# Kernel optimization log

Measured on AMD Instinct MI355X. Metric: run time of the kernel, lower is better.

The kernel has to match this reference:

```python
import jax, jax.numpy as jnp
import numpy as np

B, T, N_EMBD, HEAD = 4, 4096, 2048, 128


def setup_inputs() -> dict:
    key = jax.random.key(0)
    kx, kq, kk, kv = jax.random.split(key, 4)
    scale = 1.0 / np.sqrt(N_EMBD)
    return {
        "x": jax.random.normal(kx, (B, T, N_EMBD), dtype=jnp.float32),
        "Wq": jax.random.normal(kq, (N_EMBD, HEAD), dtype=jnp.float32) * scale,
        "Wk": jax.random.normal(kk, (N_EMBD, HEAD), dtype=jnp.float32) * scale,
        "Wv": jax.random.normal(kv, (N_EMBD, HEAD), dtype=jnp.float32) * scale,
    }


def reference(x, Wq, Wk, Wv):
    # q, k, v: [B, T, H]
    q = jnp.einsum("btn,nh->bth", x, Wq)
    k = jnp.einsum("btn,nh->bth", x, Wk)
    v = jnp.einsum("btn,nh->bth", x, Wv)
    scale = 1.0 / jnp.sqrt(jnp.asarray(HEAD, dtype=x.dtype))
    scores = jnp.einsum("bth,bsh->bts", q, k) * scale  # [B, T, T]
    causal = jnp.tril(jnp.ones((T, T), dtype=bool))
    scores = jnp.where(causal, scores, -jnp.inf)
    weights = jax.nn.softmax(scores, axis=-1)  # dropout p=0.0 -> identity
    return jnp.einsum("bts,bsh->bth", weights, v)
```

## Files before the change

kernel.cpp:

```cpp
#include <hip/hip_runtime.h>
#include <hip/hip_bf16.h>

#define B_SZ  4
#define T_SEQ 4096
#define NE    2048
#define HD    128
#define NROWS (B_SZ * T_SEQ)

typedef __attribute__((ext_vector_type(4))) float f32x4;
typedef __attribute__((ext_vector_type(8))) short s16x8;

__device__ __forceinline__ ushort f2bf(float f) {
    __hip_bfloat16 h = __float2bfloat16(f);
    return *reinterpret_cast<ushort*>(&h);
}
__device__ __forceinline__ unsigned int pk2(float a, float b) {
    return (unsigned int)f2bf(a) | ((unsigned int)f2bf(b) << 16);
}
__device__ __forceinline__ void gload_lds16(const void* g, void* l) {
    __builtin_amdgcn_global_load_lds(
        (const __attribute__((address_space(1))) unsigned int*)g,
        (__attribute__((address_space(3))) unsigned int*)l, 16, 0, 0);
}

__global__ __launch_bounds__(256) void wconv_kernel(
    const float* __restrict__ Wq, const float* __restrict__ Wk,
    const float* __restrict__ Wv, ushort* __restrict__ wt)
{
    __shared__ __align__(16) ushort tr[128][80];
    const int mat = blockIdx.y;
    const int k0  = blockIdx.x * 64;
    const float* W = (mat == 0) ? Wq : (mat == 1) ? Wk : Wv;
    const int tid = threadIdx.x;

    #pragma unroll
    for (int p = 0; p < 32; p++) {
        const int idx = p * 256 + tid;
        const int k = idx >> 7, h = idx & 127;
        tr[h][k] = f2bf(W[(size_t)(k0 + k) * HD + h]);
    }
    __syncthreads();
    const int h = tid >> 1, half = tid & 1;
    const uint4* src = (const uint4*)&tr[h][half * 32];
    uint4* dst = (uint4*)(wt + (size_t)(mat * HD + h) * NE + k0 + half * 32);
    #pragma unroll
    for (int j = 0; j < 4; j++) dst[j] = src[j];
}

__global__ __launch_bounds__(512) void qkv_kernel(
    const float* __restrict__ x, const ushort* __restrict__ wt,
    ushort* __restrict__ q_b, ushort* __restrict__ k_b, ushort* __restrict__ vt)
{
    __shared__ __align__(16) ushort xa[2][64][64];
    __shared__ __align__(16) ushort wb[2][384][64];

    const int tid  = threadIdx.x;
    const int wave = tid >> 6, lane = tid & 63;
    const int nn   = lane & 15, quad = lane >> 4;
    const int rows0 = blockIdx.x * 64;
    const int wr = (wave & 3) * 16;
    const int wc = (wave >> 2) * 192;

    f32x4 acc[12];
    #pragma unroll
    for (int nt = 0; nt < 12; nt++) acc[nt] = (f32x4){0.f, 0.f, 0.f, 0.f};

    const int srow = tid >> 3, skq = tid & 7;
    const float* xp = x + (size_t)(rows0 + srow) * NE + skq * 8;
    char* xw = (char*)&xa[0][srow][0] + ((skq * 16) ^ ((srow & 7) << 4));

    float4 xr0, xr1;
    auto load_x = [&](int kc) {
        xr0 = *(const float4*)(xp + kc);
        xr1 = *(const float4*)(xp + kc + 4);
    };
    auto write_x = [&](int buf) {
        uint4 w;
        w.x = pk2(xr0.x, xr0.y); w.y = pk2(xr0.z, xr0.w);
        w.z = pk2(xr1.x, xr1.y); w.w = pk2(xr1.z, xr1.w);
        *(uint4*)(xw + buf * 8192) = w;
    };

    const int row8 = lane >> 3, off16 = (lane & 7) * 16;
    const char* wsrc = (const char*)wt
        + (size_t)(wave * 48 + row8) * (NE * 2) + (off16 ^ (row8 << 4));
    char* wdst = (char*)&wb[0][wave * 48][0];

    auto stage_w = [&](int buf, int kc) {
        #pragma unroll
        for (int j = 0; j < 6; j++)
            gload_lds16(wsrc + (size_t)j * 8 * (NE * 2) + kc * 2,
                        wdst + buf * 49152 + j * 1024);
    };

    load_x(0);
    stage_w(0, 0);
    write_x(0);
    asm volatile("s_waitcnt vmcnt(0)" ::: "memory");
    __syncthreads();

    for (int t = 0; t < 32; t++) {
        const int kc = t * 64;
        const int cb = t & 1;
        if (t + 1 < 32) { load_x(kc + 64); stage_w(cb ^ 1, kc + 64); }
        #pragma unroll
        for (int ks = 0; ks < 2; ks++) {
            const int kb = ks * 64 + quad * 16;
            const s16x8 af = *(const s16x8*)((const char*)&xa[cb][wr + nn][0]
                                             + (kb ^ ((nn & 7) << 4)));
            #pragma unroll
            for (int nt = 0; nt < 12; nt++) {
                const int c = wc + nt * 16 + nn;
                const s16x8 bf = *(const s16x8*)((const char*)&wb[cb][c][0]
                                                 + (kb ^ ((nn & 7) << 4)));
                acc[nt] = __builtin_amdgcn_mfma_f32_16x16x32_bf16(af, bf, acc[nt], 0, 0, 0);
            }
        }
        if (t + 1 < 32) write_x(cb ^ 1);
        __syncthreads();
    }

    const float qscale = 0.08838834764831845f;
    #pragma unroll
    for (int nt = 0; nt < 12; nt++) {
        const int c = wc + nt * 16 + nn;
        #pragma unroll
        for (int r = 0; r < 4; r++) {
            const int grow = rows0 + wr + quad * 4 + r;
            const float val = acc[nt][r];
            if (c < 128)       q_b[(size_t)grow * HD + c] = f2bf(val * qscale);
            else if (c < 256)  k_b[(size_t)grow * HD + (c - 128)] = f2bf(val);
            else               vt[(size_t)(c - 256) * NROWS + grow] = f2bf(val);
        }
    }
}

__global__ __launch_bounds__(256) void attn_kernel(
    const ushort* __restrict__ q_b, const ushort* __restrict__ k_b,
    const ushort* __restrict__ vt, float* __restrict__ out)
{
    __shared__ __align__(16) char smem_raw[4 * 16 * 132 * 4];
    float (*o_smem)[16][132] = reinterpret_cast<float (*)[16][132]>(smem_raw);
    ushort (*pT)[68]         = reinterpret_cast<ushort (*)[68]>(smem_raw);
    __shared__ float l_smem[4][16];

    const int bid = blockIdx.x;
    const int xcd = bid & 7;
    const int b   = xcd >> 1;
    const int qi  = 255 - (((bid >> 3) << 1) | (xcd & 1));
    const int qrow0 = qi * 16;
    const size_t bT = (size_t)b * T_SEQ;

    const int tid  = threadIdx.x;
    const int wave = tid >> 6, lane = tid & 63;
    const int nn   = lane & 15, quad = lane >> 4;

    s16x8 qfrag[4];
    #pragma unroll
    for (int ks = 0; ks < 4; ks++)
        qfrag[ks] = *(const s16x8*)&q_b[(bT + qrow0 + nn) * HD + ks * 32 + quad * 8];

    s16x8 ones;
    #pragma unroll
    for (int j = 0; j < 8; j++) ones[j] = (short)0x3F80;

    f32x4 o_acc[8], l_acc;
    #pragma unroll
    for (int nt = 0; nt < 8; nt++) o_acc[nt] = (f32x4){0.f, 0.f, 0.f, 0.f};
    l_acc = (f32x4){0.f, 0.f, 0.f, 0.f};

    const int ntiles = (qi >> 2) + 1;

    for (int t = wave; t < ntiles; t += 4) {
        const int s0 = t * 64;
        const bool lastt = (t == ntiles - 1);

        s16x8 kf[4][4];
        #pragma unroll
        for (int ks = 0; ks < 4; ks++)
            #pragma unroll
            for (int n = 0; n < 4; n++)
                kf[ks][n] = *(const s16x8*)&k_b[(bT + s0 + n * 16 + nn) * HD + ks * 32 + quad * 8];

        f32x4 sa[4];
        #pragma unroll
        for (int n = 0; n < 4; n++) sa[n] = (f32x4){0.f, 0.f, 0.f, 0.f};
        #pragma unroll
        for (int ks = 0; ks < 4; ks++)
            #pragma unroll
            for (int n = 0; n < 4; n++)
                sa[n] = __builtin_amdgcn_mfma_f32_16x16x32_bf16(qfrag[ks], kf[ks][n], sa[n], 0, 0, 0);

        s16x8 vb[8][2];
        #pragma unroll
        for (int nt = 0; nt < 8; nt++)
            #pragma unroll
            for (int kst = 0; kst < 2; kst++)
                vb[nt][kst] = *(const s16x8*)&vt[(size_t)(nt * 16 + nn) * NROWS + bT + s0 + kst * 32 + quad * 8];

        #pragma unroll
        for (int r = 0; r < 4; r++) {
            const int grow = qrow0 + quad * 4 + r;
            #pragma unroll
            for (int n = 0; n < 4; n++) {
                const float p = (lastt && (s0 + n * 16 + nn > grow)) ? 0.0f : __expf(sa[n][r]);
                pT[wave * 16 + quad * 4 + r][n * 16 + nn] = f2bf(p);
            }
        }

        s16x8 pf[2];
        #pragma unroll
        for (int kst = 0; kst < 2; kst++)
            pf[kst] = *(const s16x8*)&pT[wave * 16 + nn][kst * 32 + quad * 8];

        #pragma unroll
        for (int kst = 0; kst < 2; kst++)
            l_acc = __builtin_amdgcn_mfma_f32_16x16x32_bf16(pf[kst], ones, l_acc, 0, 0, 0);

        #pragma unroll
        for (int nt = 0; nt < 8; nt++)
            #pragma unroll
            for (int kst = 0; kst < 2; kst++)
                o_acc[nt] = __builtin_amdgcn_mfma_f32_16x16x32_bf16(pf[kst], vb[nt][kst], o_acc[nt], 0, 0, 0);
    }

    __syncthreads();

    if (nn == 0) {
        #pragma unroll
        for (int r = 0; r < 4; r++) l_smem[wave][quad * 4 + r] = l_acc[r];
    }
    #pragma unroll
    for (int nt = 0; nt < 8; nt++)
        #pragma unroll
        for (int r = 0; r < 4; r++)
            o_smem[wave][quad * 4 + r][nt * 16 + nn] = o_acc[nt][r];

    __syncthreads();

    #pragma unroll
    for (int r = 0; r < 4; r++) {
        const int row = quad * 4 + r;
        const float L = l_smem[0][row] + l_smem[1][row] + l_smem[2][row] + l_smem[3][row];
        const float invL = 1.0f / L;
        #pragma unroll
        for (int j = 0; j < 2; j++) {
            const int col = (wave * 2 + j) * 16 + nn;
            float acc = 0.0f;
            #pragma unroll
            for (int w = 0; w < 4; w++) acc += o_smem[w][row][col];
            out[(bT + qrow0 + row) * HD + col] = acc * invL;
        }
    }
}

extern "C" void kernel_launch(void* const* d_in, const int* in_sizes, int n_in,
                              void* d_out, int out_size, void* d_ws, size_t ws_size,
                              hipStream_t stream) {
    const float* x  = (const float*)d_in[0];
    const float* Wq = (const float*)d_in[1];
    const float* Wk = (const float*)d_in[2];
    const float* Wv = (const float*)d_in[3];

    ushort* q_b = (ushort*)d_ws;
    ushort* k_b = q_b + (size_t)NROWS * HD;
    ushort* vtp = k_b + (size_t)NROWS * HD;
    ushort* wt  = vtp + (size_t)HD * NROWS;

    wconv_kernel<<<dim3(32, 3), dim3(256), 0, stream>>>(Wq, Wk, Wv, wt);
    qkv_kernel<<<dim3(256), dim3(512), 0, stream>>>(x, wt, q_b, k_b, vtp);
    attn_kernel<<<dim3(1024), dim3(256), 0, stream>>>(q_b, k_b, vtp, (float*)d_out);
}
```

Measured before the change: 361.6 us.

## Widen attention query tile to 32 rows and shrink QKV projection tiles

The attention kernel now gives each block 32 query rows (two 16-row MFMA tiles per wave), so every K and V fragment loaded from global memory feeds twice as many MFMAs, and the grid is halved to 512 blocks. The QKV projection switches to 256-thread blocks covering 32 rows with a 32-wide K step, doubling the block count to 512 and removing the XOR LDS swizzle. The attention change targets redundant K/V global loads. It costs more registers per wave and fewer blocks to balance the causal workload. The unswizzled LDS layout in the projection may cause bank conflicts, and the smaller K chunk doubles the number of barriers.

```diff
diff --git a/kernel.cpp b/kernel.cpp
--- a/kernel.cpp
+++ b/kernel.cpp
@@ -47,50 +47,42 @@
     for (int j = 0; j < 4; j++) dst[j] = src[j];
 }
 
-__global__ __launch_bounds__(512) void qkv_kernel(
+__global__ __launch_bounds__(256) void qkv_kernel(
     const float* __restrict__ x, const ushort* __restrict__ wt,
     ushort* __restrict__ q_b, ushort* __restrict__ k_b, ushort* __restrict__ vt)
 {
-    __shared__ __align__(16) ushort xa[2][64][64];
-    __shared__ __align__(16) ushort wb[2][384][64];
+    __shared__ __align__(16) ushort xa[2][32][32];
+    __shared__ __align__(16) ushort wb[2][384][32];
 
     const int tid  = threadIdx.x;
     const int wave = tid >> 6, lane = tid & 63;
     const int nn   = lane & 15, quad = lane >> 4;
-    const int rows0 = blockIdx.x * 64;
-    const int wr = (wave & 3) * 16;
-    const int wc = (wave >> 2) * 192;
+    const int rows0 = blockIdx.x * 32;
+    const int mrow  = (wave & 1) * 16;
+    const int wc    = (wave >> 1) * 192;
 
     f32x4 acc[12];
     #pragma unroll
     for (int nt = 0; nt < 12; nt++) acc[nt] = (f32x4){0.f, 0.f, 0.f, 0.f};
 
-    const int srow = tid >> 3, skq = tid & 7;
-    const float* xp = x + (size_t)(rows0 + srow) * NE + skq * 8;
-    char* xw = (char*)&xa[0][srow][0] + ((skq * 16) ^ ((srow & 7) << 4));
-
-    float4 xr0, xr1;
-    auto load_x = [&](int kc) {
-        xr0 = *(const float4*)(xp + kc);
-        xr1 = *(const float4*)(xp + kc + 4);
+    const int xrow = tid >> 3, xk = (tid & 7) * 4;
+    const float* xp = x + (size_t)(rows0 + xrow) * NE + xk;
+    float4 xr;
+    auto load_x = [&](int kc) { xr = *(const float4*)(xp + kc); };
+    auto write_x = [&](int buf) {
+        uint2 w;
+        w.x = pk2(xr.x, xr.y);
+        w.y = pk2(xr.z, xr.w);
+        *(uint2*)&xa[buf][xrow][xk] = w;
     };
-    auto write_x = [&](int buf) {
-        uint4 w;
-        w.x = pk2(xr0.x, xr0.y); w.y = pk2(xr0.z, xr0.w);
-        w.z = pk2(xr1.x, xr1.y); w.w = pk2(xr1.z, xr1.w);
-        *(uint4*)(xw + buf * 8192) = w;
-    };
-
-    const int row8 = lane >> 3, off16 = (lane & 7) * 16;
-    const char* wsrc = (const char*)wt
-        + (size_t)(wave * 48 + row8) * (NE * 2) + (off16 ^ (row8 << 4));
-    char* wdst = (char*)&wb[0][wave * 48][0];
-
+
+    const char* wsrc0 = (const char*)wt + (size_t)(tid >> 2) * (NE * 2) + (tid & 3) * 16;
+    char* wdst0 = (char*)wb + tid * 16;
     auto stage_w = [&](int buf, int kc) {
         #pragma unroll
-        for (int j = 0; j < 6; j++)
-            gload_lds16(wsrc + (size_t)j * 8 * (NE * 2) + kc * 2,
-                        wdst + buf * 49152 + j * 1024);
+        for (int rnd = 0; rnd < 6; rnd++)
+            gload_lds16(wsrc0 + (size_t)rnd * 64 * (NE * 2) + kc * 2,
+                        wdst0 + buf * 24576 + rnd * 4096);
     };
 
     load_x(0);
@@ -99,24 +91,16 @@
     asm volatile("s_waitcnt vmcnt(0)" ::: "memory");
     __syncthreads();
 
-    for (int t = 0; t < 32; t++) {
-        const int kc = t * 64;
+    for (int t = 0; t < 64; t++) {
         const int cb = t & 1;
-        if (t + 1 < 32) { load_x(kc + 64); stage_w(cb ^ 1, kc + 64); }
-        #pragma unroll
-        for (int ks = 0; ks < 2; ks++) {
-            const int kb = ks * 64 + quad * 16;
-            const s16x8 af = *(const s16x8*)((const char*)&xa[cb][wr + nn][0]
-                                             + (kb ^ ((nn & 7) << 4)));
-            #pragma unroll
-            for (int nt = 0; nt < 12; nt++) {
-                const int c = wc + nt * 16 + nn;
-                const s16x8 bf = *(const s16x8*)((const char*)&wb[cb][c][0]
-                                                 + (kb ^ ((nn & 7) << 4)));
-                acc[nt] = __builtin_amdgcn_mfma_f32_16x16x32_bf16(af, bf, acc[nt], 0, 0, 0);
-            }
-        }
-        if (t + 1 < 32) write_x(cb ^ 1);
+        if (t + 1 < 64) { load_x((t + 1) * 32); stage_w(cb ^ 1, (t + 1) * 32); }
+        const s16x8 af = *(const s16x8*)&xa[cb][mrow + nn][quad * 8];
+        #pragma unroll
+        for (int nt = 0; nt < 12; nt++) {
+            const s16x8 bf = *(const s16x8*)&wb[cb][wc + nt * 16 + nn][quad * 8];
+            acc[nt] = __builtin_amdgcn_mfma_f32_16x16x32_bf16(af, bf, acc[nt], 0, 0, 0);
+        }
+        if (t + 1 < 64) write_x(cb ^ 1);
         __syncthreads();
     }
 
@@ -126,7 +110,7 @@
         const int c = wc + nt * 16 + nn;
         #pragma unroll
         for (int r = 0; r < 4; r++) {
-            const int grow = rows0 + wr + quad * 4 + r;
+            const int grow = rows0 + mrow + quad * 4 + r;
             const float val = acc[nt][r];
             if (c < 128)       q_b[(size_t)grow * HD + c] = f2bf(val * qscale);
             else if (c < 256)  k_b[(size_t)grow * HD + (c - 128)] = f2bf(val);
@@ -139,37 +123,42 @@
     const ushort* __restrict__ q_b, const ushort* __restrict__ k_b,
     const ushort* __restrict__ vt, float* __restrict__ out)
 {
-    __shared__ __align__(16) char smem_raw[4 * 16 * 132 * 4];
-    float (*o_smem)[16][132] = reinterpret_cast<float (*)[16][132]>(smem_raw);
+    __shared__ __align__(16) char smem_raw[4 * 32 * 132 * 4];
+    float (*o_smem)[32][132] = reinterpret_cast<float (*)[32][132]>(smem_raw);
     ushort (*pT)[68]         = reinterpret_cast<ushort (*)[68]>(smem_raw);
-    __shared__ float l_smem[4][16];
+    __shared__ float l_smem[4][32];
 
     const int bid = blockIdx.x;
     const int xcd = bid & 7;
     const int b   = xcd >> 1;
-    const int qi  = 255 - (((bid >> 3) << 1) | (xcd & 1));
-    const int qrow0 = qi * 16;
+    const int qi  = 127 - (((bid >> 3) << 1) | (xcd & 1));
+    const int qrow0 = qi * 32;
     const size_t bT = (size_t)b * T_SEQ;
 
     const int tid  = threadIdx.x;
     const int wave = tid >> 6, lane = tid & 63;
     const int nn   = lane & 15, quad = lane >> 4;
 
-    s16x8 qfrag[4];
-    #pragma unroll
-    for (int ks = 0; ks < 4; ks++)
-        qfrag[ks] = *(const s16x8*)&q_b[(bT + qrow0 + nn) * HD + ks * 32 + quad * 8];
+    s16x8 qfrag[2][4];
+    #pragma unroll
+    for (int m = 0; m < 2; m++)
+        #pragma unroll
+        for (int ks = 0; ks < 4; ks++)
+            qfrag[m][ks] = *(const s16x8*)&q_b[(bT + qrow0 + m * 16 + nn) * HD + ks * 32 + quad * 8];
 
     s16x8 ones;
     #pragma unroll
     for (int j = 0; j < 8; j++) ones[j] = (short)0x3F80;
 
-    f32x4 o_acc[8], l_acc;
-    #pragma unroll
-    for (int nt = 0; nt < 8; nt++) o_acc[nt] = (f32x4){0.f, 0.f, 0.f, 0.f};
-    l_acc = (f32x4){0.f, 0.f, 0.f, 0.f};
-
-    const int ntiles = (qi >> 2) + 1;
+    f32x4 o_acc[2][8], l_acc[2];
+    #pragma unroll
+    for (int m = 0; m < 2; m++) {
+        #pragma unroll
+        for (int nt = 0; nt < 8; nt++) o_acc[m][nt] = (f32x4){0.f, 0.f, 0.f, 0.f};
+        l_acc[m] = (f32x4){0.f, 0.f, 0.f, 0.f};
+    }
+
+    const int ntiles = (qi >> 1) + 1;
 
     for (int t = wave; t < ntiles; t += 4) {
         const int s0 = t * 64;
@@ -182,14 +171,19 @@
             for (int n = 0; n < 4; n++)
                 kf[ks][n] = *(const s16x8*)&k_b[(bT + s0 + n * 16 + nn) * HD + ks * 32 + quad * 8];
 
-        f32x4 sa[4];
-        #pragma unroll
-        for (int n = 0; n < 4; n++) sa[n] = (f32x4){0.f, 0.f, 0.f, 0.f};
+        f32x4 sa[2][4];
+        #pragma unroll
+        for (int m = 0; m < 2; m++)
+            #pragma unroll
+            for (int n = 0; n < 4; n++) sa[m][n] = (f32x4){0.f, 0.f, 0.f, 0.f};
         #pragma unroll
         for (int ks = 0; ks < 4; ks++)
             #pragma unroll
             for (int n = 0; n < 4; n++)
-                sa[n] = __builtin_amdgcn_mfma_f32_16x16x32_bf16(qfrag[ks], kf[ks][n], sa[n], 0, 0, 0);
+                #pragma unroll
+                for (int m = 0; m < 2; m++)
+                    sa[m][n] = __builtin_amdgcn_mfma_f32_16x16x32_bf16(
+                        qfrag[m][ks], kf[ks][n], sa[m][n], 0, 0, 0);
 
         s16x8 vb[8][2];
         #pragma unroll
@@ -199,59 +193,74 @@
                 vb[nt][kst] = *(const s16x8*)&vt[(size_t)(nt * 16 + nn) * NROWS + bT + s0 + kst * 32 + quad * 8];
 
         #pragma unroll
-        for (int r = 0; r < 4; r++) {
-            const int grow = qrow0 + quad * 4 + r;
-            #pragma unroll
-            for (int n = 0; n < 4; n++) {
-                const float p = (lastt && (s0 + n * 16 + nn > grow)) ? 0.0f : __expf(sa[n][r]);
-                pT[wave * 16 + quad * 4 + r][n * 16 + nn] = f2bf(p);
+        for (int m = 0; m < 2; m++)
+            #pragma unroll
+            for (int r = 0; r < 4; r++) {
+                const int grow = qrow0 + m * 16 + quad * 4 + r;
+                #pragma unroll
+                for (int n = 0; n < 4; n++) {
+                    const float p = (lastt && (s0 + n * 16 + nn > grow)) ? 0.0f : __expf(sa[m][n][r]);
+                    pT[wave * 32 + m * 16 + quad * 4 + r][n * 16 + nn] = f2bf(p);
+                }
             }
-        }
-
-        s16x8 pf[2];
-        #pragma unroll
-        for (int kst = 0; kst < 2; kst++)
-            pf[kst] = *(const s16x8*)&pT[wave * 16 + nn][kst * 32 + quad * 8];
-
-        #pragma unroll
-        for (int kst = 0; kst < 2; kst++)
-            l_acc = __builtin_amdgcn_mfma_f32_16x16x32_bf16(pf[kst], ones, l_acc, 0, 0, 0);
+
+        s16x8 pf[2][2];
+        #pragma unroll
+        for (int m = 0; m < 2; m++)
+            #pragma unroll
+            for (int kst = 0; kst < 2; kst++)
+                pf[m][kst] = *(const s16x8*)&pT[wave * 32 + m * 16 + nn][kst * 32 + quad * 8];
+
+        #pragma unroll
+        for (int m = 0; m < 2; m++)
+            #pragma unroll
+            for (int kst = 0; kst < 2; kst++)
+                l_acc[m] = __builtin_amdgcn_mfma_f32_16x16x32_bf16(pf[m][kst], ones, l_acc[m], 0, 0, 0);
 
         #pragma unroll
         for (int nt = 0; nt < 8; nt++)
             #pragma unroll
             for (int kst = 0; kst < 2; kst++)
-                o_acc[nt] = __builtin_amdgcn_mfma_f32_16x16x32_bf16(pf[kst], vb[nt][kst], o_acc[nt], 0, 0, 0);
-    }
-
-    __syncthreads();
-
-    if (nn == 0) {
-        #pragma unroll
-        for (int r = 0; r < 4; r++) l_smem[wave][quad * 4 + r] = l_acc[r];
-    }
-    #pragma unroll
-    for (int nt = 0; nt < 8; nt++)
-        #pragma unroll
-        for (int r = 0; r < 4; r++)
-            o_smem[wave][quad * 4 + r][nt * 16 + nn] = o_acc[nt][r];
-
-    __syncthreads();
-
-    #pragma unroll
-    for (int r = 0; r < 4; r++) {
-        const int row = quad * 4 + r;
-        const float L = l_smem[0][row] + l_smem[1][row] + l_smem[2][row] + l_smem[3][row];
-        const float invL = 1.0f / L;
-        #pragma unroll
-        for (int j = 0; j < 2; j++) {
-            const int col = (wave * 2 + j) * 16 + nn;
-            float acc = 0.0f;
-            #pragma unroll
-            for (int w = 0; w < 4; w++) acc += o_smem[w][row][col];
-            out[(bT + qrow0 + row) * HD + col] = acc * invL;
-        }
-    }
+                #pragma unroll
+                for (int m = 0; m < 2; m++)
+                    o_acc[m][nt] = __builtin_amdgcn_mfma_f32_16x16x32_bf16(
+                        pf[m][kst], vb[nt][kst], o_acc[m][nt], 0, 0, 0);
+    }
+
+    __syncthreads();
+
+    #pragma unroll
+    for (int m = 0; m < 2; m++) {
+        if (nn == 0) {
+            #pragma unroll
+            for (int r = 0; r < 4; r++)
+                l_smem[wave][m * 16 + quad * 4 + r] = l_acc[m][r];
+        }
+        #pragma unroll
+        for (int nt = 0; nt < 8; nt++)
+            #pragma unroll
+            for (int r = 0; r < 4; r++)
+                o_smem[wave][m * 16 + quad * 4 + r][nt * 16 + nn] = o_acc[m][nt][r];
+    }
+
+    __syncthreads();
+
+    #pragma unroll
+    for (int half = 0; half < 2; half++)
+        #pragma unroll
+        for (int rr = 0; rr < 4; rr++) {
+            const int row = half * 16 + quad * 4 + rr;
+            const float L = l_smem[0][row] + l_smem[1][row] + l_smem[2][row] + l_smem[3][row];
+            const float invL = 1.0f / L;
+            #pragma unroll
+            for (int j = 0; j < 2; j++) {
+                const int col = wave * 32 + j * 16 + nn;
+                float s = 0.0f;
+                #pragma unroll
+                for (int p = 0; p < 4; p++) s += o_smem[p][row][col];
+                out[(bT + qrow0 + row) * HD + col] = s * invL;
+            }
+        }
 }
 
 extern "C" void kernel_launch(void* const* d_in, const int* in_sizes, int n_in,
@@ -268,6 +277,6 @@
     ushort* wt  = vtp + (size_t)HD * NROWS;
 
     wconv_kernel<<<dim3(32, 3), dim3(256), 0, stream>>>(Wq, Wk, Wv, wt);
-    qkv_kernel<<<dim3(256), dim3(512), 0, stream>>>(x, wt, q_b, k_b, vtp);
-    attn_kernel<<<dim3(1024), dim3(256), 0, stream>>>(q_b, k_b, vtp, (float*)d_out);
-}
+    qkv_kernel<<<dim3(512), dim3(256), 0, stream>>>(x, wt, q_b, k_b, vtp);
+    attn_kernel<<<dim3(512), dim3(256), 0, stream>>>(q_b, k_b, vtp, (float*)d_out);
+}
```

Result: faster. 334.1 us (-7.6%).
